# Kernel optimization log

Hardware: AMD Instinct MI355X
Metric: run time of the kernel (lower is better)

## Reference

```python
import jax, jax.numpy as jnp
import numpy as np

B, L, D = 16384, 6, 256
LN_EPS = 1e-5


def _layernorm(x, gamma, beta):
    mu = jnp.mean(x, axis=-1, keepdims=True)
    var = jnp.mean(jnp.square(x - mu), axis=-1, keepdims=True)
    return (x - mu) * jax.lax.rsqrt(var + LN_EPS) * gamma + beta


def _mlp_block(x, W, b, ln_g, ln_b):
    # Linear(D, D) -> LayerNorm(D) -> ReLU
    return jax.nn.relu(_layernorm(x @ W + b, ln_g, ln_b))


def setup_inputs() -> dict:
    key = jax.random.key(0)
    ks = jax.random.split(key, 8)
    s = 1.0 / np.sqrt(D)
    return {
        "gfeat": jax.random.normal(ks[0], (B, L, D), jnp.float32),
        "pfeat": jax.random.normal(ks[1], (B, L, D), jnp.float32),
        "Wg": jax.random.normal(ks[2], (D, D), jnp.float32) * s,
        "bg": jax.random.normal(ks[3], (D,), jnp.float32) * s,
        "g_ln_g": jnp.ones((D,), jnp.float32),
        "g_ln_b": jnp.zeros((D,), jnp.float32),
        "Wp": jax.random.normal(ks[4], (D, D), jnp.float32) * s,
        "bp": jax.random.normal(ks[5], (D,), jnp.float32) * s,
        "p_ln_g": jnp.ones((D,), jnp.float32),
        "p_ln_b": jnp.zeros((D,), jnp.float32),
        "wa_g": jax.random.normal(ks[6], (D,), jnp.float32) * s,
        "ba_g": jnp.zeros((), jnp.float32),
        "wa_p": jax.random.normal(ks[7], (D,), jnp.float32) * s,
        "ba_p": jnp.zeros((), jnp.float32),
    }


def reference(gfeat, pfeat, Wg, bg, g_ln_g, g_ln_b, Wp, bp, p_ln_g, p_ln_b,
              wa_g, ba_g, wa_p, ba_p):
    # g_align, p_align: [B, L, D]
    g_align = _mlp_block(gfeat, Wg, bg, g_ln_g, g_ln_b)
    p_align = _mlp_block(pfeat, Wp, bp, p_ln_g, p_ln_b)

    # Original torch code materializes atten[b,l,i,j] = g_align[b,l,i] * p_align[b,l,j]
    # ([B,L,D,D]) then applies Linear(D,1)+sigmoid along j (geno) / along i (path).
    # Mathematically:
    #   geno_att[b,l,i] = sigmoid(g_align[b,l,i] * (p_align[b,l] @ wa_g) + ba_g)
    #   path_att[b,l,j] = sigmoid(p_align[b,l,j] * (g_align[b,l] @ wa_p) + ba_p)
    # so we compute the bilinear reduction without forming the 4D tensor.
    p_red = jnp.einsum('bld,d->bl', p_align, wa_g)[..., None]  # [B,L,1]
    g_red = jnp.einsum('bld,d->bl', g_align, wa_p)[..., None]  # [B,L,1]
    geno_att = jax.nn.sigmoid(g_align * p_red + ba_g)
    path_att = jax.nn.sigmoid(p_align * g_red + ba_p)

    interaction = p_align * path_att + g_align * geno_att  # [B,L,D]
    return interaction
```

## Files before the change

### kernel.cpp

```cpp
#include <hip/hip_runtime.h>
#include <hip/hip_bf16.h>


typedef float f32x4 __attribute__((ext_vector_type(4)));
typedef short short8 __attribute__((ext_vector_type(8)));
typedef unsigned int u32;

#define D_DIM 256
#define ROWS 16
#define NW 4

union S8 { short8 s; u32 u[4]; };

__device__ __forceinline__ u32 f2bfu(float x) {
  u32 u = __float_as_uint(x);
  return (u + 0x7FFFu + ((u >> 16) & 1u)) >> 16;
}
__device__ __forceinline__ float sigm(float x) { return 1.0f / (1.0f + __expf(-x)); }

__device__ __forceinline__ u32 pk2c(float a, float b) {
  __hip_bfloat162 h = __float22bfloat162_rn(float2{a, b});
  union { __hip_bfloat162 h; u32 u; } cv;
  cv.h = h;
  return cv.u;
}

__global__ __launch_bounds__(256) void pack_w_kernel(const float* __restrict__ Wg,
                                                     const float* __restrict__ Wp,
                                                     unsigned short* __restrict__ outp) {
  int b = blockIdx.x;
  const float* W = (b < 32) ? Wg : Wp;
  unsigned short* o = outp + (b < 32 ? 0 : 65536);
  int chunk = (b & 31) * 256 + threadIdx.x;
  int c = chunk >> 9;
  int rest = chunk & 511;
  int t = rest >> 6;
  int l = rest & 63;
  int m = c * 16 + (l & 15);
  int kb = t * 32 + ((l >> 4) << 3);
  short8 v;
#pragma unroll
  for (int j = 0; j < 8; ++j) v[j] = (short)f2bfu(W[(kb + j) * 256 + m]);
  *(short8*)(o + (size_t)chunk * 8) = v;
}


__device__ __forceinline__ void stage_dma(const float* __restrict__ src, float* lbuf,
                                          int w, int lane) {
#pragma unroll
  for (int j = 0; j < 4; ++j) {
    int r = w * 4 + j;
    const float* gp = src + r * D_DIM + ((lane ^ (r & 7)) << 2);
    float* lp = lbuf + r * D_DIM;
    __builtin_amdgcn_global_load_lds(
        (const __attribute__((address_space(1))) u32*)gp,
        (__attribute__((address_space(3))) u32*)lp, 16, 0, 0);
  }
}

__device__ __forceinline__ void barrier_fence() {
  __builtin_amdgcn_s_barrier();
  asm volatile("" ::: "memory");
}

__device__ __forceinline__ short8 readAf32(const float* buf, int t, int lane) {
  const int cl = lane & 15, kg = lane >> 4;
  const int r = cl;
  const int s = r & 7;
  const int c16 = t * 8 + kg * 2;
  const char* base = (const char*)buf + r * 1024;
  float4 x = *(const float4*)(base + ((c16 ^ s) << 4));
  float4 y = *(const float4*)(base + (((c16 + 1) ^ s) << 4));
  S8 rr;
  rr.u[0] = pk2c(x.x, x.y);
  rr.u[1] = pk2c(x.z, x.w);
  rr.u[2] = pk2c(y.x, y.y);
  rr.u[3] = pk2c(y.z, y.w);
  return rr.s;
}

__device__ __forceinline__ void gemm4(f32x4 acc[4], const float* buf,
                                      const short8* __restrict__ wb, int lane, int w) {
  const int bbase = w * 2048 + lane;
#pragma unroll
  for (int h = 0; h < 2; ++h) {
    short8 a[4];
#pragma unroll
    for (int tt = 0; tt < 4; ++tt) a[tt] = readAf32(buf, h * 4 + tt, lane);
#pragma unroll
    for (int c = 0; c < 4; ++c) {
      short8 bf[4];
#pragma unroll
      for (int tt = 0; tt < 4; ++tt) bf[tt] = wb[bbase + c * 512 + (h * 4 + tt) * 64];
#pragma unroll
      for (int tt = 0; tt < 4; ++tt)
        acc[c] = __builtin_amdgcn_mfma_f32_16x16x32_bf16(a[tt], bf[tt], acc[c], 0, 0, 0);
    }
  }
}

__device__ __forceinline__ void statsPhase(f32x4 acc[4], const float bv[4],
                                           float smS[NW][ROWS], float smQ[NW][ROWS],
                                           int lane, int w) {
#pragma unroll
  for (int r = 0; r < 4; ++r) {
    float s = 0.f, qq = 0.f;
#pragma unroll
    for (int c = 0; c < 4; ++c) {
      float y = acc[c][r] + bv[c];
      acc[c][r] = y;
      s += y; qq += y * y;
    }
#pragma unroll
    for (int m = 1; m < 16; m <<= 1) {
      s += __shfl_xor(s, m, 64);
      qq += __shfl_xor(qq, m, 64);
    }
    if ((lane & 15) == 0) {
      int row = ((lane >> 4) << 2) + r;
      smS[w][row] = s;
      smQ[w][row] = qq;
    }
  }
}

__device__ __forceinline__ void applyPhase(f32x4 acc[4], f32x4 outAl[4],
                                           const float gv[4], const float tv[4], const float wv[4],
                                           const float smS[NW][ROWS], const float smQ[NW][ROWS],
                                           float smRed[NW][ROWS], int lane, int w) {
#pragma unroll
  for (int r = 0; r < 4; ++r) {
    int row = ((lane >> 4) << 2) + r;
    float s = 0.f, qq = 0.f;
#pragma unroll
    for (int k = 0; k < NW; ++k) { s += smS[k][row]; qq += smQ[k][row]; }
    float mu = s * (1.0f / 256.0f);
    float var = fmaxf(qq * (1.0f / 256.0f) - mu * mu, 0.0f);
    float rs = rsqrtf(var + 1e-5f);
    float dp = 0.f;
#pragma unroll
    for (int c = 0; c < 4; ++c) {
      float a = (acc[c][r] - mu) * rs * gv[c] + tv[c];
      a = fmaxf(a, 0.0f);
      outAl[c][r] = a;
      dp += a * wv[c];
    }
#pragma unroll
    for (int m = 1; m < 16; m <<= 1) dp += __shfl_xor(dp, m, 64);
    if ((lane & 15) == 0) smRed[w][row] = dp;
  }
}

__global__ __launch_bounds__(256, 4) void fused_main(
    const float* __restrict__ gfeat, const float* __restrict__ pfeat,
    const float* __restrict__ bg, const float* __restrict__ glng, const float* __restrict__ glnb,
    const float* __restrict__ bp, const float* __restrict__ plng, const float* __restrict__ plnb,
    const float* __restrict__ wag, const float* __restrict__ bag,
    const float* __restrict__ wap, const float* __restrict__ bap,
    const unsigned short* __restrict__ wpk,
    float* __restrict__ outp)
{
  __shared__ float bufG[ROWS * D_DIM];
  __shared__ float bufP[ROWS * D_DIM];
  __shared__ float smSG[NW][ROWS], smQG[NW][ROWS];
  __shared__ float smSP[NW][ROWS], smQP[NW][ROWS];
  __shared__ float smRG[NW][ROWS], smRP[NW][ROWS];

  const int tid = threadIdx.x;
  const int lane = tid & 63;
  const int w = tid >> 6;
  const size_t row0 = (size_t)blockIdx.x * ROWS;

  const short8* wbg = (const short8*)wpk;
  const short8* wbp = (const short8*)(wpk + 65536);

  stage_dma(gfeat + row0 * D_DIM, bufG, w, lane);
  stage_dma(pfeat + row0 * D_DIM, bufP, w, lane);

  const int cb = w * 64 + (lane & 15);
  float bvG[4], bvP[4];
#pragma unroll
  for (int c = 0; c < 4; ++c) {
    bvG[c] = bg[cb + c * 16];
    bvP[c] = bp[cb + c * 16];
  }
  const float vbag = bag[0], vbap = bap[0];

  asm volatile("s_waitcnt vmcnt(0)" ::: "memory");
  barrier_fence();

  f32x4 accG[4], accP[4];
#pragma unroll
  for (int c = 0; c < 4; ++c) {
    accG[c] = {0.f, 0.f, 0.f, 0.f};
    accP[c] = {0.f, 0.f, 0.f, 0.f};
  }
  gemm4(accG, bufG, wbg, lane, w);
  gemm4(accP, bufP, wbp, lane, w);

  float gvG[4], tvG[4], wvG[4], gvP[4], tvP[4], wvP[4];
#pragma unroll
  for (int c = 0; c < 4; ++c) {
    gvG[c] = glng[cb + c * 16];
    tvG[c] = glnb[cb + c * 16];
    wvG[c] = wap[cb + c * 16];
    gvP[c] = plng[cb + c * 16];
    tvP[c] = plnb[cb + c * 16];
    wvP[c] = wag[cb + c * 16];
  }

  statsPhase(accG, bvG, smSG, smQG, lane, w);
  statsPhase(accP, bvP, smSP, smQP, lane, w);
  asm volatile("s_waitcnt lgkmcnt(0)" ::: "memory");
  barrier_fence();

  f32x4 alignG[4];
  applyPhase(accG, alignG, gvG, tvG, wvG, smSG, smQG, smRG, lane, w);
  applyPhase(accP, accP,   gvP, tvP, wvP, smSP, smQP, smRP, lane, w);
  asm volatile("s_waitcnt lgkmcnt(0)" ::: "memory");
  barrier_fence();

#pragma unroll
  for (int r = 0; r < 4; ++r) {
    int row = ((lane >> 4) << 2) + r;
    float gr = 0.f, pr = 0.f;
#pragma unroll
    for (int k = 0; k < NW; ++k) { gr += smRG[k][row]; pr += smRP[k][row]; }
    float* orow = outp + (row0 + row) * D_DIM + w * 64 + (lane & 15);
#pragma unroll
    for (int c = 0; c < 4; ++c) {
      float ga = alignG[c][r];
      float pa = accP[c][r];
      float geno = sigm(ga * pr + vbag);
      float path = sigm(pa * gr + vbap);
      orow[c * 16] = pa * path + ga * geno;
    }
  }
}

extern "C" void kernel_launch(void* const* d_in, const int* in_sizes, int n_in,
                              void* d_out, int out_size, void* d_ws, size_t ws_size,
                              hipStream_t stream) {
  const float* gfeat = (const float*)d_in[0];
  const float* pfeat = (const float*)d_in[1];
  const float* Wg   = (const float*)d_in[2];
  const float* bg   = (const float*)d_in[3];
  const float* glng = (const float*)d_in[4];
  const float* glnb = (const float*)d_in[5];
  const float* Wp   = (const float*)d_in[6];
  const float* bp   = (const float*)d_in[7];
  const float* plng = (const float*)d_in[8];
  const float* plnb = (const float*)d_in[9];
  const float* wag  = (const float*)d_in[10];
  const float* bag  = (const float*)d_in[11];
  const float* wap  = (const float*)d_in[12];
  const float* bap  = (const float*)d_in[13];
  float* outp = (float*)d_out;
  unsigned short* wpk = (unsigned short*)d_ws;

  hipLaunchKernelGGL(pack_w_kernel, dim3(64), dim3(256), 0, stream, Wg, Wp, wpk);

  int nrows = in_sizes[0] / D_DIM;
  int nblocks = nrows / ROWS;
  hipLaunchKernelGGL(fused_main, dim3(nblocks), dim3(256), 0, stream,
                     gfeat, pfeat, bg, glng, glnb, bp, plng, plnb,
                     wag, bag, wap, bap, wpk, outp);
}
```

Before: 136.0 us.

## Stream packed weights through double-buffered LDS and serialize the G and P GEMMs

Packed bf16 weight fragments are now fetched per wave into a double-buffered LDS region with async global-to-LDS loads, instead of being read straight from global memory into registers inside the MFMA loop. The two GEMMs now run one after the other: a single activation buffer first holds gfeat, then is refilled with pfeat while the G branch's LayerNorm is applied. This is meant to overlap weight fetch with MFMA work and hide the pfeat load behind G-side compute. In exchange it adds vmcnt-based waits, extra barriers and a longer serial chain. The weight buffers also raise total LDS use, which may lower occupancy. A refilled weight buffer is not explicitly guarded against LDS reads that may still be in flight.

```diff
diff --git a/kernel.cpp b/kernel.cpp
--- a/kernel.cpp
+++ b/kernel.cpp
@@ -24,6 +24,9 @@
   cv.h = h;
   return cv.u;
 }
+
+#define WAITV(n) asm volatile("s_waitcnt vmcnt(" #n ")" ::: "memory")
+#define WAITL    asm volatile("s_waitcnt lgkmcnt(0)" ::: "memory")
 
 __global__ __launch_bounds__(256) void pack_w_kernel(const float* __restrict__ Wg,
                                                      const float* __restrict__ Wp,
@@ -58,6 +61,18 @@
   }
 }
 
+__device__ __forceinline__ void w_dma(const unsigned short* __restrict__ wsrc,
+                                      unsigned short* wdst, int w, int t, int lane) {
+#pragma unroll
+  for (int j = 0; j < 4; ++j) {
+    const unsigned short* gp = wsrc + (((w * 4 + j) * 512 + t * 64 + lane) << 3);
+    unsigned short* lp = wdst + j * 512;
+    __builtin_amdgcn_global_load_lds(
+        (const __attribute__((address_space(1))) u32*)gp,
+        (__attribute__((address_space(3))) u32*)lp, 16, 0, 0);
+  }
+}
+
 __device__ __forceinline__ void barrier_fence() {
   __builtin_amdgcn_s_barrier();
   asm volatile("" ::: "memory");
@@ -79,26 +94,6 @@
   return rr.s;
 }
 
-__device__ __forceinline__ void gemm4(f32x4 acc[4], const float* buf,
-                                      const short8* __restrict__ wb, int lane, int w) {
-  const int bbase = w * 2048 + lane;
-#pragma unroll
-  for (int h = 0; h < 2; ++h) {
-    short8 a[4];
-#pragma unroll
-    for (int tt = 0; tt < 4; ++tt) a[tt] = readAf32(buf, h * 4 + tt, lane);
-#pragma unroll
-    for (int c = 0; c < 4; ++c) {
-      short8 bf[4];
-#pragma unroll
-      for (int tt = 0; tt < 4; ++tt) bf[tt] = wb[bbase + c * 512 + (h * 4 + tt) * 64];
-#pragma unroll
-      for (int tt = 0; tt < 4; ++tt)
-        acc[c] = __builtin_amdgcn_mfma_f32_16x16x32_bf16(a[tt], bf[tt], acc[c], 0, 0, 0);
-    }
-  }
-}
-
 __device__ __forceinline__ void statsPhase(f32x4 acc[4], const float bv[4],
                                            float smS[NW][ROWS], float smQ[NW][ROWS],
                                            int lane, int w) {
@@ -160,22 +155,21 @@
     const unsigned short* __restrict__ wpk,
     float* __restrict__ outp)
 {
-  __shared__ float bufG[ROWS * D_DIM];
-  __shared__ float bufP[ROWS * D_DIM];
-  __shared__ float smSG[NW][ROWS], smQG[NW][ROWS];
-  __shared__ float smSP[NW][ROWS], smQP[NW][ROWS];
-  __shared__ float smRG[NW][ROWS], smRP[NW][ROWS];
+  __shared__ float bufA[ROWS * D_DIM];
+  __shared__ unsigned short smW[NW][2][2048];
+  __shared__ float smS[NW][ROWS], smQ[NW][ROWS], smRG[NW][ROWS], smRP[NW][ROWS];
 
   const int tid = threadIdx.x;
   const int lane = tid & 63;
   const int w = tid >> 6;
   const size_t row0 = (size_t)blockIdx.x * ROWS;
 
-  const short8* wbg = (const short8*)wpk;
-  const short8* wbp = (const short8*)(wpk + 65536);
-
-  stage_dma(gfeat + row0 * D_DIM, bufG, w, lane);
-  stage_dma(pfeat + row0 * D_DIM, bufP, w, lane);
+  const unsigned short* wgS = wpk;
+  const unsigned short* wpS = wpk + 65536;
+
+  stage_dma(gfeat + row0 * D_DIM, bufA, w, lane);
+  w_dma(wgS, &smW[w][0][0], w, 0, lane);
+  w_dma(wgS, &smW[w][1][0], w, 1, lane);
 
   const int cb = w * 64 + (lane & 15);
   float bvG[4], bvP[4];
@@ -186,17 +180,33 @@
   }
   const float vbag = bag[0], vbap = bap[0];
 
-  asm volatile("s_waitcnt vmcnt(0)" ::: "memory");
-  barrier_fence();
-
-  f32x4 accG[4], accP[4];
-#pragma unroll
-  for (int c = 0; c < 4; ++c) {
-    accG[c] = {0.f, 0.f, 0.f, 0.f};
-    accP[c] = {0.f, 0.f, 0.f, 0.f};
-  }
-  gemm4(accG, bufG, wbg, lane, w);
-  gemm4(accP, bufP, wbp, lane, w);
+  WAITV(8);
+  barrier_fence();
+
+  f32x4 accG[4];
+#pragma unroll
+  for (int c = 0; c < 4; ++c) accG[c] = {0.f, 0.f, 0.f, 0.f};
+
+#pragma unroll
+  for (int t = 0; t < 8; ++t) {
+    WAITV(4);
+    short8 a = readAf32(bufA, t, lane);
+    const unsigned short* wl = &smW[w][t & 1][0];
+#pragma unroll
+    for (int c = 0; c < 4; ++c) {
+      short8 b = *(const short8*)(wl + c * 512 + lane * 8);
+      accG[c] = __builtin_amdgcn_mfma_f32_16x16x32_bf16(a, b, accG[c], 0, 0, 0);
+    }
+    __builtin_amdgcn_sched_barrier(0);
+    if (t < 6) w_dma(wgS, &smW[w][t & 1][0], w, t + 2, lane);
+    else       w_dma(wpS, &smW[w][t & 1][0], w, t - 6, lane);
+  }
+
+  statsPhase(accG, bvG, smS, smQ, lane, w);
+  WAITL;
+  barrier_fence();
+
+  stage_dma(pfeat + row0 * D_DIM, bufA, w, lane);
 
   float gvG[4], tvG[4], wvG[4], gvP[4], tvP[4], wvP[4];
 #pragma unroll
@@ -209,15 +219,37 @@
     wvP[c] = wag[cb + c * 16];
   }
 
-  statsPhase(accG, bvG, smSG, smQG, lane, w);
-  statsPhase(accP, bvP, smSP, smQP, lane, w);
-  asm volatile("s_waitcnt lgkmcnt(0)" ::: "memory");
-  barrier_fence();
-
   f32x4 alignG[4];
-  applyPhase(accG, alignG, gvG, tvG, wvG, smSG, smQG, smRG, lane, w);
-  applyPhase(accP, accP,   gvP, tvP, wvP, smSP, smQP, smRP, lane, w);
-  asm volatile("s_waitcnt lgkmcnt(0)" ::: "memory");
+  applyPhase(accG, alignG, gvG, tvG, wvG, smS, smQ, smRG, lane, w);
+  WAITV(0);
+  WAITL;
+  barrier_fence();
+
+  f32x4 accP[4];
+#pragma unroll
+  for (int c = 0; c < 4; ++c) accP[c] = {0.f, 0.f, 0.f, 0.f};
+
+#pragma unroll
+  for (int t = 0; t < 8; ++t) {
+    if (t >= 1 && t <= 6) { WAITV(4); }
+    else if (t == 7)      { WAITV(0); }
+    short8 a = readAf32(bufA, t, lane);
+    const unsigned short* wl = &smW[w][t & 1][0];
+#pragma unroll
+    for (int c = 0; c < 4; ++c) {
+      short8 b = *(const short8*)(wl + c * 512 + lane * 8);
+      accP[c] = __builtin_amdgcn_mfma_f32_16x16x32_bf16(a, b, accP[c], 0, 0, 0);
+    }
+    __builtin_amdgcn_sched_barrier(0);
+    if (t < 6) w_dma(wpS, &smW[w][t & 1][0], w, t + 2, lane);
+  }
+
+  statsPhase(accP, bvP, smS, smQ, lane, w);
+  WAITL;
+  barrier_fence();
+
+  applyPhase(accP, accP, gvP, tvP, wvP, smS, smQ, smRP, lane, w);
+  WAITL;
   barrier_fence();
 
 #pragma unroll
```

Result: slower. 151.3 us (+11.2%).

## Load GEMM A operands straight from global memory and serialize G/P paths

Applied to the files above, without the earlier changes.

Drops the LDS staging of the gfeat/pfeat tiles through global_load_lds and has each wave read its A fragments as float4 loads directly from global memory. The G and P branches are now run one after the other (GEMM, stats, barrier, apply) instead of side by side. This frees 32KB of LDS per block, which may raise occupancy and allows the P GEMM to overlap the G apply phase. The cost is that every wave reloads the same A rows from global memory or cache, in an uncoalesced, strided pattern.

```diff
diff --git a/kernel.cpp b/kernel.cpp
--- a/kernel.cpp
+++ b/kernel.cpp
@@ -24,6 +24,8 @@
   cv.h = h;
   return cv.u;
 }
+
+#define WAITL asm volatile("s_waitcnt lgkmcnt(0)" ::: "memory")
 
 __global__ __launch_bounds__(256) void pack_w_kernel(const float* __restrict__ Wg,
                                                      const float* __restrict__ Wp,
@@ -45,32 +47,16 @@
 }
 
 
-__device__ __forceinline__ void stage_dma(const float* __restrict__ src, float* lbuf,
-                                          int w, int lane) {
-#pragma unroll
-  for (int j = 0; j < 4; ++j) {
-    int r = w * 4 + j;
-    const float* gp = src + r * D_DIM + ((lane ^ (r & 7)) << 2);
-    float* lp = lbuf + r * D_DIM;
-    __builtin_amdgcn_global_load_lds(
-        (const __attribute__((address_space(1))) u32*)gp,
-        (__attribute__((address_space(3))) u32*)lp, 16, 0, 0);
-  }
-}
-
 __device__ __forceinline__ void barrier_fence() {
   __builtin_amdgcn_s_barrier();
   asm volatile("" ::: "memory");
 }
 
-__device__ __forceinline__ short8 readAf32(const float* buf, int t, int lane) {
+__device__ __forceinline__ short8 ldAg(const float* __restrict__ A, int t, int lane) {
   const int cl = lane & 15, kg = lane >> 4;
-  const int r = cl;
-  const int s = r & 7;
-  const int c16 = t * 8 + kg * 2;
-  const char* base = (const char*)buf + r * 1024;
-  float4 x = *(const float4*)(base + ((c16 ^ s) << 4));
-  float4 y = *(const float4*)(base + (((c16 + 1) ^ s) << 4));
+  const float* p = A + cl * D_DIM + kg * 8 + t * 32;
+  float4 x = *(const float4*)p;
+  float4 y = *(const float4*)(p + 4);
   S8 rr;
   rr.u[0] = pk2c(x.x, x.y);
   rr.u[1] = pk2c(x.z, x.w);
@@ -79,14 +65,14 @@
   return rr.s;
 }
 
-__device__ __forceinline__ void gemm4(f32x4 acc[4], const float* buf,
+__device__ __forceinline__ void gemm4(f32x4 acc[4], const float* __restrict__ A,
                                       const short8* __restrict__ wb, int lane, int w) {
   const int bbase = w * 2048 + lane;
 #pragma unroll
   for (int h = 0; h < 2; ++h) {
     short8 a[4];
 #pragma unroll
-    for (int tt = 0; tt < 4; ++tt) a[tt] = readAf32(buf, h * 4 + tt, lane);
+    for (int tt = 0; tt < 4; ++tt) a[tt] = ldAg(A, h * 4 + tt, lane);
 #pragma unroll
     for (int c = 0; c < 4; ++c) {
       short8 bf[4];
@@ -160,8 +146,6 @@
     const unsigned short* __restrict__ wpk,
     float* __restrict__ outp)
 {
-  __shared__ float bufG[ROWS * D_DIM];
-  __shared__ float bufP[ROWS * D_DIM];
   __shared__ float smSG[NW][ROWS], smQG[NW][ROWS];
   __shared__ float smSP[NW][ROWS], smQP[NW][ROWS];
   __shared__ float smRG[NW][ROWS], smRP[NW][ROWS];
@@ -173,9 +157,8 @@
 
   const short8* wbg = (const short8*)wpk;
   const short8* wbp = (const short8*)(wpk + 65536);
-
-  stage_dma(gfeat + row0 * D_DIM, bufG, w, lane);
-  stage_dma(pfeat + row0 * D_DIM, bufP, w, lane);
+  const float* Ag = gfeat + row0 * D_DIM;
+  const float* Ap = pfeat + row0 * D_DIM;
 
   const int cb = w * 64 + (lane & 15);
   float bvG[4], bvP[4];
@@ -186,17 +169,13 @@
   }
   const float vbag = bag[0], vbap = bap[0];
 
-  asm volatile("s_waitcnt vmcnt(0)" ::: "memory");
+  f32x4 accG[4];
+#pragma unroll
+  for (int c = 0; c < 4; ++c) accG[c] = {0.f, 0.f, 0.f, 0.f};
+  gemm4(accG, Ag, wbg, lane, w);
+  statsPhase(accG, bvG, smSG, smQG, lane, w);
+  WAITL;
   barrier_fence();
-
-  f32x4 accG[4], accP[4];
-#pragma unroll
-  for (int c = 0; c < 4; ++c) {
-    accG[c] = {0.f, 0.f, 0.f, 0.f};
-    accP[c] = {0.f, 0.f, 0.f, 0.f};
-  }
-  gemm4(accG, bufG, wbg, lane, w);
-  gemm4(accP, bufP, wbp, lane, w);
 
   float gvG[4], tvG[4], wvG[4], gvP[4], tvP[4], wvP[4];
 #pragma unroll
@@ -209,15 +188,19 @@
     wvP[c] = wag[cb + c * 16];
   }
 
-  statsPhase(accG, bvG, smSG, smQG, lane, w);
-  statsPhase(accP, bvP, smSP, smQP, lane, w);
-  asm volatile("s_waitcnt lgkmcnt(0)" ::: "memory");
-  barrier_fence();
-
   f32x4 alignG[4];
   applyPhase(accG, alignG, gvG, tvG, wvG, smSG, smQG, smRG, lane, w);
-  applyPhase(accP, accP,   gvP, tvP, wvP, smSP, smQP, smRP, lane, w);
-  asm volatile("s_waitcnt lgkmcnt(0)" ::: "memory");
+
+  f32x4 accP[4];
+#pragma unroll
+  for (int c = 0; c < 4; ++c) accP[c] = {0.f, 0.f, 0.f, 0.f};
+  gemm4(accP, Ap, wbp, lane, w);
+  statsPhase(accP, bvP, smSP, smQP, lane, w);
+  WAITL;
+  barrier_fence();
+
+  applyPhase(accP, accP, gvP, tvP, wvP, smSP, smQP, smRP, lane, w);
+  WAITL;
   barrier_fence();
 
 #pragma unroll
```

Measured after the change: 207.8 us. +52.7%, slower.
